# Optimization experiments

Measured on AMD Instinct MI355X. Metric: run time of the kernel, lower is better.

Reference implementation:

```python
import jax, jax.numpy as jnp
import numpy as np

B, N, DIN, H, DOUT = 32, 1024, 256, 256, 256
NEG = 9000000000000000.0  # -9e15 masking trick from the original code


def setup_inputs() -> dict:
    key = jax.random.key(0)
    ks = jax.random.split(key, 10)
    x = jax.random.normal(ks[0], (B, N, DIN), dtype=jnp.float32)
    # binary float mask (1 = edge present)
    mask = jax.random.randint(ks[1], (B, N, N), 0, 2).astype(jnp.float32)
    s = 0.02
    Wv = jax.random.normal(ks[2], (DIN, H), dtype=jnp.float32) * s
    bv = jnp.zeros((H,), jnp.float32)
    Wk = jax.random.normal(ks[3], (DIN, H), dtype=jnp.float32) * s
    bk = jnp.zeros((H,), jnp.float32)
    Wq = jax.random.normal(ks[4], (DIN, H), dtype=jnp.float32) * s
    bq = jnp.zeros((H,), jnp.float32)
    Wo = jax.random.normal(ks[5], (H, DOUT), dtype=jnp.float32) * s
    bo = jnp.zeros((DOUT,), jnp.float32)
    return {"x": x, "mask": mask, "Wv": Wv, "bv": bv, "Wk": Wk, "bk": bk,
            "Wq": Wq, "bq": bq, "Wo": Wo, "bo": bo}


def reference(x, mask, Wv, bv, Wk, bk, Wq, bq, Wo, bo):
    # x: [B,N,din], mask: [B,N,N]
    v = jax.nn.relu(x @ Wv + bv)              # [B,N,H]
    q = jax.nn.relu(x @ Wq + bq)              # [B,N,H]
    k = jax.nn.relu(x @ Wk + bk)              # [B,N,H]
    scores = jnp.einsum('bnh,bmh->bnm', q, k)  # QK^T, [B,N,N]
    att = jax.nn.softmax(scores * mask - NEG * (1.0 - mask), axis=-1)
    out = jnp.einsum('bnm,bmh->bnh', att, v)   # AV
    return jax.nn.relu(out @ Wo + bo)          # [B,N,d_out]
```

## Files before the change

kernel.cpp:

```cpp
#include <hip/hip_runtime.h>


typedef __attribute__((ext_vector_type(4))) float    f32x4;
typedef __attribute__((ext_vector_type(8))) short    s16x8;
typedef __attribute__((ext_vector_type(4))) short    s16x4;
typedef unsigned long long u64;

__device__ __forceinline__ short f2b(float f) {
    union { float f; unsigned u; } v; v.f = f;
    unsigned r = v.u + 0x7FFFu + ((v.u >> 16) & 1u);
    return (short)(r >> 16);
}

__device__ __forceinline__ void gl_lds16(const short* g, short* l) {
    __builtin_amdgcn_global_load_lds(
        (const __attribute__((address_space(1))) unsigned int*)g,
        (__attribute__((address_space(3))) unsigned int*)l, 16, 0, 0);
}

__global__ void prep_w(const float* __restrict__ Wq, const float* __restrict__ Wk,
                       const float* __restrict__ Wv, const float* __restrict__ Wo,
                       short* __restrict__ Wt) {
    int idx = blockIdx.x * 256 + threadIdx.x;
    int w = idx >> 16, rem = idx & 65535;
    int n = rem >> 8, kk = rem & 255;
    const float* W = (w == 0) ? Wq : (w == 1) ? Wk : (w == 2) ? Wv : Wo;
    Wt[idx] = f2b(W[kk * 256 + n]);
}

__global__ __launch_bounds__(256) void qkv_gemm(
        const float* __restrict__ x, const short* __restrict__ Wt,
        const float* __restrict__ bq, const float* __restrict__ bk, const float* __restrict__ bv,
        short* __restrict__ qO, short* __restrict__ kO, short* __restrict__ vtO) {
    __shared__ short a_lds[128][72];
    __shared__ short b_lds[3][64][72];
    const int tid = threadIdx.x;
    const int bm = blockIdx.x >> 2, bn = blockIdx.x & 3;
    const int s0 = bm * 128, n0 = bn * 64;
    const int wid = tid >> 6, l = tid & 63, lo4 = l & 15, hi4 = l >> 4;
    const int wm = wid >> 1, wn = wid & 1;

    f32x4 acc[3][4][2];
    #pragma unroll
    for (int w = 0; w < 3; ++w)
        #pragma unroll
        for (int mi = 0; mi < 4; ++mi)
            #pragma unroll
            for (int ni = 0; ni < 2; ++ni)
                acc[w][mi][ni] = (f32x4){0.f, 0.f, 0.f, 0.f};

    for (int kt = 0; kt < 4; ++kt) {
        const int k0 = kt * 64;
        #pragma unroll
        for (int i = 0; i < 8; ++i) {
            int ch = i * 256 + tid;
            int row = ch >> 4, c4 = (ch & 15) * 4;
            f32x4 xv = *(const f32x4*)(x + (size_t)(s0 + row) * 256 + k0 + c4);
            s16x4 pk = { f2b(xv.x), f2b(xv.y), f2b(xv.z), f2b(xv.w) };
            *(s16x4*)&a_lds[row][c4] = pk;
        }
        #pragma unroll
        for (int w = 0; w < 3; ++w) {
            #pragma unroll
            for (int i = 0; i < 2; ++i) {
                int ch = i * 256 + tid;
                int n = ch >> 3, c8 = (ch & 7) * 8;
                *(s16x8*)&b_lds[w][n][c8] =
                    *(const s16x8*)(Wt + (size_t)w * 65536 + (size_t)(n0 + n) * 256 + k0 + c8);
            }
        }
        __syncthreads();
        s16x8 af[4][2];
        #pragma unroll
        for (int mi = 0; mi < 4; ++mi)
            #pragma unroll
            for (int kk = 0; kk < 2; ++kk)
                af[mi][kk] = *(s16x8*)&a_lds[wm * 64 + mi * 16 + lo4][kk * 32 + hi4 * 8];
        #pragma unroll
        for (int w = 0; w < 3; ++w)
            #pragma unroll
            for (int ni = 0; ni < 2; ++ni)
                #pragma unroll
                for (int kk = 0; kk < 2; ++kk) {
                    s16x8 bfr = *(s16x8*)&b_lds[w][wn * 32 + ni * 16 + lo4][kk * 32 + hi4 * 8];
                    #pragma unroll
                    for (int mi = 0; mi < 4; ++mi)
                        acc[w][mi][ni] = __builtin_amdgcn_mfma_f32_16x16x32_bf16(
                            af[mi][kk], bfr, acc[w][mi][ni], 0, 0, 0);
                }
        __syncthreads();
    }

    const float* bias[3] = { bq, bk, bv };
    for (int w = 0; w < 3; ++w) {
        #pragma unroll
        for (int mi = 0; mi < 4; ++mi)
            #pragma unroll
            for (int ni = 0; ni < 2; ++ni)
                #pragma unroll
                for (int j = 0; j < 4; ++j) {
                    int r = wm * 64 + mi * 16 + hi4 * 4 + j;
                    int c = wn * 32 + ni * 16 + lo4;
                    float v = acc[w][mi][ni][j] + bias[w][n0 + c];
                    a_lds[r][c] = f2b(fmaxf(v, 0.f));
                }
        __syncthreads();
        if (w == 0) {
            #pragma unroll
            for (int i = 0; i < 4; ++i) {
                int ch = i * 256 + tid;
                int row = ch >> 3, c8 = (ch & 7) * 8;
                *(s16x8*)(qO + (size_t)(s0 + row) * 256 + n0 + c8) = *(s16x8*)&a_lds[row][c8];
            }
        } else if (w == 1) {
            #pragma unroll
            for (int i = 0; i < 4; ++i) {
                int ch = i * 256 + tid;
                int row = ch >> 3, c8 = (ch & 7) * 8;
                int swz = ((c8 >> 3) ^ (row & 7)) * 8;
                *(s16x8*)(kO + (size_t)(s0 + row) * 256 + n0 + swz) = *(s16x8*)&a_lds[row][c8];
            }
        } else {
            int bb = s0 >> 10, nn = s0 & 1023;
            #pragma unroll
            for (int i = 0; i < 4; ++i) {
                int ch = i * 256 + tid;
                int h = ch >> 4, sc = (ch & 15) * 8;
                s16x8 t;
                #pragma unroll
                for (int e = 0; e < 8; ++e) t[e] = a_lds[sc + e][h];
                int cil = sc >> 3;
                int swz = (cil & 8) | ((cil & 7) ^ ((n0 + h) & 7));
                *(s16x8*)(vtO + ((size_t)bb * 256 + n0 + h) * 1024 + nn + swz * 8) = t;
            }
        }
        __syncthreads();
    }
}

__global__ __launch_bounds__(512) void attn_fused(
        const short* __restrict__ q, const short* __restrict__ k,
        const short* __restrict__ vt, const float* __restrict__ mask,
        const short* __restrict__ WtO, const float* __restrict__ bo,
        float* __restrict__ out) {
    __shared__ short SM[65536];
    __shared__ short p_lds[8][16][72];
    const int tid = threadIdx.x, wid = tid >> 6, l = tid & 63;
    const int lo4 = l & 15, hi4 = l >> 4;
    const int bid = blockIdx.x;
    const int swz = (bid & 7) * 32 + (bid >> 3);
    const int b = swz >> 3, qb = swz & 7;
    const int q0 = qb * 128 + wid * 16;
    const size_t bq0 = (size_t)b * 1024 + qb * 128;
    const size_t bq_row = (size_t)b * 1024 + q0;

    const short* kb  = k  + (size_t)b * 1024 * 256;
    const short* vtg = vt + (size_t)b * 256 * 1024;
    const float* mtb = mask + bq_row * 1024;

#define KBUF(bufi) (SM + (bufi) * 16384)
#define VBUF(bufi) (SM + 32768 + (bufi) * 16384)
#define STAGE_K(bufi, c0_) do { const short* sg_ = kb + (size_t)(c0_) * 256;          \
    _Pragma("unroll") for (int i_ = 0; i_ < 4; ++i_) { int cb_ = i_ * 512 + wid * 64; \
        gl_lds16(sg_ + (size_t)(cb_ + l) * 8, KBUF(bufi) + cb_ * 8); } } while (0)
#define STAGE_V(bufi, c0_) do {                                                       \
    _Pragma("unroll") for (int i_ = 0; i_ < 4; ++i_) { int cb_ = i_ * 512 + wid * 64; \
        int ch_ = cb_ + l; int h_ = ch_ >> 3, cc_ = ch_ & 7;                          \
        gl_lds16(vtg + (size_t)h_ * 1024 + (c0_) + cc_ * 8, VBUF(bufi) + cb_ * 8); } } while (0)
#define LOAD_MASK(dst, c0_) do {                                                      \
    _Pragma("unroll") for (int i_ = 0; i_ < 4; ++i_)                                  \
        dst[i_] = *(const f32x4*)(mtb + (size_t)(i_ * 4 + hi4) * 1024 + (c0_) + lo4 * 4); } while (0)

    s16x8 qf[8];
    {
        const short* qp = q + (bq_row + lo4) * 256 + hi4 * 8;
        #pragma unroll
        for (int t = 0; t < 8; ++t) qf[t] = *(const s16x8*)(qp + t * 32);
    }
    f32x4 oacc[16];
    #pragma unroll
    for (int t = 0; t < 16; ++t) oacc[t] = (f32x4){0.f, 0.f, 0.f, 0.f};
    float m_run[4] = { -1e30f, -1e30f, -1e30f, -1e30f };
    float l_run[4] = { 0.f, 0.f, 0.f, 0.f };
    f32x4 mk0[4], mk1[4], mk2[4];

    LOAD_MASK(mk0, 0);
    STAGE_K(0, 0);
    STAGE_V(0, 0);
    LOAD_MASK(mk1, 64);

    for (int t = 0; t < 16; ++t) {
        const int cur = t & 1;
        const int c0 = t * 64;
        if (t < 15) {
            STAGE_K(cur ^ 1, c0 + 64);
            asm volatile("s_waitcnt vmcnt(12)" ::: "memory");
        } else {
            asm volatile("s_waitcnt vmcnt(4)" ::: "memory");
        }
        __builtin_amdgcn_s_barrier();
        f32x4 s[4];
        #pragma unroll
        for (int ct = 0; ct < 4; ++ct) s[ct] = (f32x4){0.f, 0.f, 0.f, 0.f};
        __builtin_amdgcn_s_setprio(1);
        #pragma unroll
        for (int ct = 0; ct < 4; ++ct) {
            int row = ct * 16 + lo4, rx = row & 7;
            #pragma unroll
            for (int tt = 0; tt < 8; ++tt) {
                int ch = tt * 4 + hi4;
                int sc = (ch & 24) | ((ch & 7) ^ rx);
                s16x8 kf = *(s16x8*)(KBUF(cur) + row * 256 + sc * 8);
                s[ct] = __builtin_amdgcn_mfma_f32_16x16x32_bf16(qf[tt], kf, s[ct], 0, 0, 0);
            }
        }
        __builtin_amdgcn_s_setprio(0);
        u64 bw[4][4];
        #pragma unroll
        for (int i = 0; i < 4; ++i) {
            bw[i][0] = __ballot(mk0[i].x != 0.f);
            bw[i][1] = __ballot(mk0[i].y != 0.f);
            bw[i][2] = __ballot(mk0[i].z != 0.f);
            bw[i][3] = __ballot(mk0[i].w != 0.f);
        }
        const int cc = lo4 & 3;
        u64 w0 = (cc == 0) ? bw[0][0] : (cc == 1) ? bw[0][1] : (cc == 2) ? bw[0][2] : bw[0][3];
        u64 w1 = (cc == 0) ? bw[1][0] : (cc == 1) ? bw[1][1] : (cc == 2) ? bw[1][2] : bw[1][3];
        u64 w2 = (cc == 0) ? bw[2][0] : (cc == 1) ? bw[2][1] : (cc == 2) ? bw[2][2] : bw[2][3];
        u64 w3 = (cc == 0) ? bw[3][0] : (cc == 1) ? bw[3][1] : (cc == 2) ? bw[3][2] : bw[3][3];
        u64 wsel = (hi4 == 0) ? w0 : (hi4 == 1) ? w1 : (hi4 == 2) ? w2 : w3;
        const unsigned sh0 = (unsigned)(lo4 >> 2);
        float sm[4][4];
        #pragma unroll
        for (int j = 0; j < 4; ++j) {
            unsigned wsx = (unsigned)(wsel >> (j * 16 + sh0));
            sm[0][j] = (wsx & 1u)    ? s[0][j] : -1e30f;
            sm[1][j] = (wsx & 16u)   ? s[1][j] : -1e30f;
            sm[2][j] = (wsx & 256u)  ? s[2][j] : -1e30f;
            sm[3][j] = (wsx & 4096u) ? s[3][j] : -1e30f;
        }
        float scale[4], p[4][4];
        #pragma unroll
        for (int j = 0; j < 4; ++j) {
            float tmx = fmaxf(fmaxf(sm[0][j], sm[1][j]), fmaxf(sm[2][j], sm[3][j]));
            tmx = fmaxf(tmx, __shfl_xor(tmx, 1));
            tmx = fmaxf(tmx, __shfl_xor(tmx, 2));
            tmx = fmaxf(tmx, __shfl_xor(tmx, 4));
            tmx = fmaxf(tmx, __shfl_xor(tmx, 8));
            float mnew = fmaxf(m_run[j], tmx);
            scale[j] = __expf(m_run[j] - mnew);
            m_run[j] = mnew;
            float su = 0.f;
            #pragma unroll
            for (int ct = 0; ct < 4; ++ct) { p[ct][j] = __expf(sm[ct][j] - mnew); su += p[ct][j]; }
            su += __shfl_xor(su, 1);
            su += __shfl_xor(su, 2);
            su += __shfl_xor(su, 4);
            su += __shfl_xor(su, 8);
            l_run[j] = l_run[j] * scale[j] + su;
        }
        #pragma unroll
        for (int tt = 0; tt < 16; ++tt)
            #pragma unroll
            for (int j = 0; j < 4; ++j) oacc[tt][j] *= scale[j];
        #pragma unroll
        for (int ct = 0; ct < 4; ++ct)
            #pragma unroll
            for (int j = 0; j < 4; ++j)
                p_lds[wid][hi4 * 4 + j][ct * 16 + lo4] = f2b(p[ct][j]);
        asm volatile("s_waitcnt lgkmcnt(0)" ::: "memory");
        __builtin_amdgcn_sched_barrier(0);
        s16x8 pa0 = *(s16x8*)&p_lds[wid][lo4][hi4 * 8];
        s16x8 pa1 = *(s16x8*)&p_lds[wid][lo4][32 + hi4 * 8];
        if (t < 15) {
            STAGE_V(cur ^ 1, c0 + 64);
            if (t < 14) {
                LOAD_MASK(mk2, c0 + 128);
                asm volatile("s_waitcnt vmcnt(16)" ::: "memory");
            } else {
                asm volatile("s_waitcnt vmcnt(12)" ::: "memory");
            }
        } else {
            asm volatile("s_waitcnt vmcnt(0)" ::: "memory");
        }
        __builtin_amdgcn_s_barrier();
        __builtin_amdgcn_s_setprio(1);
        #pragma unroll
        for (int nt = 0; nt < 16; ++nt) {
            int h = nt * 16 + lo4, hx = h & 7;
            s16x8 vf0 = *(s16x8*)(VBUF(cur) + h * 64 + (hi4 ^ hx) * 8);
            s16x8 vf1 = *(s16x8*)(VBUF(cur) + h * 64 + ((hi4 + 4) ^ hx) * 8);
            oacc[nt] = __builtin_amdgcn_mfma_f32_16x16x32_bf16(pa0, vf0, oacc[nt], 0, 0, 0);
            oacc[nt] = __builtin_amdgcn_mfma_f32_16x16x32_bf16(pa1, vf1, oacc[nt], 0, 0, 0);
        }
        __builtin_amdgcn_s_setprio(0);
        if (t < 15) {
            #pragma unroll
            for (int i = 0; i < 4; ++i) { mk0[i] = mk1[i]; mk1[i] = mk2[i]; }
        }
    }
    __syncthreads();

    float inv[4];
    #pragma unroll
    for (int j = 0; j < 4; ++j) inv[j] = 1.f / l_run[j];
    #pragma unroll
    for (int g = 0; g < 4; ++g) {
        asm volatile("s_waitcnt lgkmcnt(0)" ::: "memory");
        #pragma unroll
        for (int ntl = 0; ntl < 4; ++ntl)
            #pragma unroll
            for (int j = 0; j < 4; ++j)
                p_lds[wid][hi4 * 4 + j][ntl * 16 + lo4] = f2b(oacc[g * 4 + ntl][j] * inv[j]);
        asm volatile("s_waitcnt lgkmcnt(0)" ::: "memory");
        __builtin_amdgcn_sched_barrier(0);
        s16x8 r0 = *(s16x8*)&p_lds[wid][lo4][hi4 * 16];
        s16x8 r1 = *(s16x8*)&p_lds[wid][lo4][hi4 * 16 + 8];
        int arow = wid * 16 + lo4;
        *(s16x8*)&SM[arow * 264 + g * 64 + hi4 * 16]     = r0;
        *(s16x8*)&SM[arow * 264 + g * 64 + hi4 * 16 + 8] = r1;
    }
    short* wo = SM + 33792;
    #pragma unroll
    for (int i = 0; i < 4; ++i) {
        int idx = i * 512 + tid;
        int n = idx >> 5, c8 = (idx & 31) * 8;
        *(s16x8*)&wo[n * 264 + c8] = *(const s16x8*)(WtO + (size_t)n * 256 + c8);
    }
    __syncthreads();

    for (int chk = 0; chk < 4; ++chk) {
        const int n0 = chk * 64;
        f32x4 acc2[4];
        #pragma unroll
        for (int ni = 0; ni < 4; ++ni) acc2[ni] = (f32x4){0.f, 0.f, 0.f, 0.f};
        #pragma unroll
        for (int kk = 0; kk < 8; ++kk) {
            s16x8 af = *(s16x8*)&SM[(wid * 16 + lo4) * 264 + kk * 32 + hi4 * 8];
            #pragma unroll
            for (int ni = 0; ni < 4; ++ni) {
                s16x8 bf = *(s16x8*)&wo[(ni * 16 + lo4) * 264 + kk * 32 + hi4 * 8];
                acc2[ni] = __builtin_amdgcn_mfma_f32_16x16x32_bf16(af, bf, acc2[ni], 0, 0, 0);
            }
        }
        #pragma unroll
        for (int ni = 0; ni < 4; ++ni) {
            float bv = bo[n0 + ni * 16 + lo4];
            #pragma unroll
            for (int j = 0; j < 4; ++j) {
                int r = wid * 16 + hi4 * 4 + j;
                out[(bq0 + r) * 256 + n0 + ni * 16 + lo4] = fmaxf(acc2[ni][j] + bv, 0.f);
            }
        }
        if (chk < 3) {
            __syncthreads();
            #pragma unroll
            for (int i = 0; i < 4; ++i) {
                int idx = i * 512 + tid;
                int n = idx >> 5, c8 = (idx & 31) * 8;
                *(s16x8*)&wo[n * 264 + c8] =
                    *(const s16x8*)(WtO + (size_t)(n0 + 64 + n) * 256 + c8);
            }
            __syncthreads();
        }
    }
#undef KBUF
#undef VBUF
#undef STAGE_K
#undef STAGE_V
#undef LOAD_MASK
}

extern "C" void kernel_launch(void* const* d_in, const int* in_sizes, int n_in,
                              void* d_out, int out_size, void* d_ws, size_t ws_size,
                              hipStream_t stream) {
    const float* x    = (const float*)d_in[0];
    const float* mask = (const float*)d_in[1];
    const float* Wv   = (const float*)d_in[2];
    const float* bv   = (const float*)d_in[3];
    const float* Wk   = (const float*)d_in[4];
    const float* bk   = (const float*)d_in[5];
    const float* Wq   = (const float*)d_in[6];
    const float* bq   = (const float*)d_in[7];
    const float* Wo   = (const float*)d_in[8];
    const float* bo   = (const float*)d_in[9];
    float* out = (float*)d_out;

    char* ws = (char*)d_ws;
    short* Wt   = (short*)ws;
    short* qB   = (short*)(ws + (1 << 20));
    short* kB   = qB  + (size_t)32768 * 256;
    short* vtB  = kB  + (size_t)32768 * 256;
    (void)in_sizes; (void)n_in; (void)out_size; (void)ws_size;

    prep_w<<<1024, 256, 0, stream>>>(Wq, Wk, Wv, Wo, Wt);
    qkv_gemm<<<1024, 256, 0, stream>>>(x, Wt, bq, bk, bv, qB, kB, vtB);
    attn_fused<<<256, 512, 0, stream>>>(qB, kB, vtB, mask, Wt + 3 * 65536, bo, out);
}
```

Before: 125.1 us.

## Halve attention block size and single-buffer K/V to raise occupancy

```diff
diff --git a/kernel.cpp b/kernel.cpp
--- a/kernel.cpp
+++ b/kernel.cpp
@@ -138,38 +138,43 @@
     }
 }
 
-__global__ __launch_bounds__(512) void attn_fused(
+__global__ __launch_bounds__(256) void attn_fused(
         const short* __restrict__ q, const short* __restrict__ k,
         const short* __restrict__ vt, const float* __restrict__ mask,
         const short* __restrict__ WtO, const float* __restrict__ bo,
         float* __restrict__ out) {
-    __shared__ short SM[65536];
-    __shared__ short p_lds[8][16][72];
+    __shared__ short kbuf[16384];
+    __shared__ short vbuf[16384];
+    __shared__ short p_lds[4][16][72];
     const int tid = threadIdx.x, wid = tid >> 6, l = tid & 63;
     const int lo4 = l & 15, hi4 = l >> 4;
     const int bid = blockIdx.x;
-    const int swz = (bid & 7) * 32 + (bid >> 3);
-    const int b = swz >> 3, qb = swz & 7;
-    const int q0 = qb * 128 + wid * 16;
-    const size_t bq0 = (size_t)b * 1024 + qb * 128;
+    const int swz = (bid & 7) * 64 + (bid >> 3);
+    const int b = swz >> 4, qb = swz & 15;
+    const int q0 = qb * 64 + wid * 16;
+    const size_t bq0 = (size_t)b * 1024 + qb * 64;
     const size_t bq_row = (size_t)b * 1024 + q0;
 
     const short* kb  = k  + (size_t)b * 1024 * 256;
     const short* vtg = vt + (size_t)b * 256 * 1024;
     const float* mtb = mask + bq_row * 1024;
 
-#define KBUF(bufi) (SM + (bufi) * 16384)
-#define VBUF(bufi) (SM + 32768 + (bufi) * 16384)
-#define STAGE_K(bufi, c0_) do { const short* sg_ = kb + (size_t)(c0_) * 256;          \
-    _Pragma("unroll") for (int i_ = 0; i_ < 4; ++i_) { int cb_ = i_ * 512 + wid * 64; \
-        gl_lds16(sg_ + (size_t)(cb_ + l) * 8, KBUF(bufi) + cb_ * 8); } } while (0)
-#define STAGE_V(bufi, c0_) do {                                                       \
-    _Pragma("unroll") for (int i_ = 0; i_ < 4; ++i_) { int cb_ = i_ * 512 + wid * 64; \
+#define STAGE_K(c0_) do { const short* sg_ = kb + (size_t)(c0_) * 256;                \
+    _Pragma("unroll") for (int i_ = 0; i_ < 8; ++i_) { int cb_ = i_ * 256 + wid * 64; \
+        gl_lds16(sg_ + (size_t)(cb_ + l) * 8, kbuf + cb_ * 8); } } while (0)
+#define STAGE_V(c0_) do {                                                             \
+    _Pragma("unroll") for (int i_ = 0; i_ < 8; ++i_) { int cb_ = i_ * 256 + wid * 64; \
         int ch_ = cb_ + l; int h_ = ch_ >> 3, cc_ = ch_ & 7;                          \
-        gl_lds16(vtg + (size_t)h_ * 1024 + (c0_) + cc_ * 8, VBUF(bufi) + cb_ * 8); } } while (0)
+        gl_lds16(vtg + (size_t)h_ * 1024 + (c0_) + cc_ * 8, vbuf + cb_ * 8); } } while (0)
 #define LOAD_MASK(dst, c0_) do {                                                      \
     _Pragma("unroll") for (int i_ = 0; i_ < 4; ++i_)                                  \
         dst[i_] = *(const f32x4*)(mtb + (size_t)(i_ * 4 + hi4) * 1024 + (c0_) + lo4 * 4); } while (0)
+
+    f32x4 mk0[4], mk1[4], mk2[4];
+    LOAD_MASK(mk0, 0);
+    STAGE_K(0);
+    STAGE_V(0);
+    LOAD_MASK(mk1, 64);
 
     s16x8 qf[8];
     {
@@ -182,22 +187,11 @@
     for (int t = 0; t < 16; ++t) oacc[t] = (f32x4){0.f, 0.f, 0.f, 0.f};
     float m_run[4] = { -1e30f, -1e30f, -1e30f, -1e30f };
     float l_run[4] = { 0.f, 0.f, 0.f, 0.f };
-    f32x4 mk0[4], mk1[4], mk2[4];
-
-    LOAD_MASK(mk0, 0);
-    STAGE_K(0, 0);
-    STAGE_V(0, 0);
-    LOAD_MASK(mk1, 64);
 
     for (int t = 0; t < 16; ++t) {
-        const int cur = t & 1;
         const int c0 = t * 64;
-        if (t < 15) {
-            STAGE_K(cur ^ 1, c0 + 64);
-            asm volatile("s_waitcnt vmcnt(12)" ::: "memory");
-        } else {
-            asm volatile("s_waitcnt vmcnt(4)" ::: "memory");
-        }
+        if (t < 15) { asm volatile("s_waitcnt vmcnt(4)" ::: "memory"); }
+        else        { asm volatile("s_waitcnt vmcnt(0)" ::: "memory"); }
         __builtin_amdgcn_s_barrier();
         f32x4 s[4];
         #pragma unroll
@@ -210,11 +204,13 @@
             for (int tt = 0; tt < 8; ++tt) {
                 int ch = tt * 4 + hi4;
                 int sc = (ch & 24) | ((ch & 7) ^ rx);
-                s16x8 kf = *(s16x8*)(KBUF(cur) + row * 256 + sc * 8);
+                s16x8 kf = *(s16x8*)&kbuf[row * 256 + sc * 8];
                 s[ct] = __builtin_amdgcn_mfma_f32_16x16x32_bf16(qf[tt], kf, s[ct], 0, 0, 0);
             }
         }
         __builtin_amdgcn_s_setprio(0);
+        __builtin_amdgcn_s_barrier();
+        if (t < 15) STAGE_K(c0 + 64);
         u64 bw[4][4];
         #pragma unroll
         for (int i = 0; i < 4; ++i) {
@@ -272,38 +268,29 @@
         __builtin_amdgcn_sched_barrier(0);
         s16x8 pa0 = *(s16x8*)&p_lds[wid][lo4][hi4 * 8];
         s16x8 pa1 = *(s16x8*)&p_lds[wid][lo4][32 + hi4 * 8];
-        if (t < 15) {
-            STAGE_V(cur ^ 1, c0 + 64);
-            if (t < 14) {
-                LOAD_MASK(mk2, c0 + 128);
-                asm volatile("s_waitcnt vmcnt(16)" ::: "memory");
-            } else {
-                asm volatile("s_waitcnt vmcnt(12)" ::: "memory");
-            }
-        } else {
-            asm volatile("s_waitcnt vmcnt(0)" ::: "memory");
-        }
-        __builtin_amdgcn_s_barrier();
         __builtin_amdgcn_s_setprio(1);
         #pragma unroll
         for (int nt = 0; nt < 16; ++nt) {
             int h = nt * 16 + lo4, hx = h & 7;
-            s16x8 vf0 = *(s16x8*)(VBUF(cur) + h * 64 + (hi4 ^ hx) * 8);
-            s16x8 vf1 = *(s16x8*)(VBUF(cur) + h * 64 + ((hi4 + 4) ^ hx) * 8);
+            s16x8 vf0 = *(s16x8*)&vbuf[h * 64 + (hi4 ^ hx) * 8];
+            s16x8 vf1 = *(s16x8*)&vbuf[h * 64 + ((hi4 + 4) ^ hx) * 8];
             oacc[nt] = __builtin_amdgcn_mfma_f32_16x16x32_bf16(pa0, vf0, oacc[nt], 0, 0, 0);
             oacc[nt] = __builtin_amdgcn_mfma_f32_16x16x32_bf16(pa1, vf1, oacc[nt], 0, 0, 0);
         }
         __builtin_amdgcn_s_setprio(0);
+        __builtin_amdgcn_s_barrier();
         if (t < 15) {
+            STAGE_V(c0 + 64);
+            if (t < 14) LOAD_MASK(mk2, c0 + 128);
             #pragma unroll
             for (int i = 0; i < 4; ++i) { mk0[i] = mk1[i]; mk1[i] = mk2[i]; }
         }
     }
-    __syncthreads();
 
     float inv[4];
     #pragma unroll
     for (int j = 0; j < 4; ++j) inv[j] = 1.f / l_run[j];
+    s16x8 af2[8];
     #pragma unroll
     for (int g = 0; g < 4; ++g) {
         asm volatile("s_waitcnt lgkmcnt(0)" ::: "memory");
@@ -314,58 +301,45 @@
                 p_lds[wid][hi4 * 4 + j][ntl * 16 + lo4] = f2b(oacc[g * 4 + ntl][j] * inv[j]);
         asm volatile("s_waitcnt lgkmcnt(0)" ::: "memory");
         __builtin_amdgcn_sched_barrier(0);
-        s16x8 r0 = *(s16x8*)&p_lds[wid][lo4][hi4 * 16];
-        s16x8 r1 = *(s16x8*)&p_lds[wid][lo4][hi4 * 16 + 8];
-        int arow = wid * 16 + lo4;
-        *(s16x8*)&SM[arow * 264 + g * 64 + hi4 * 16]     = r0;
-        *(s16x8*)&SM[arow * 264 + g * 64 + hi4 * 16 + 8] = r1;
-    }
-    short* wo = SM + 33792;
-    #pragma unroll
-    for (int i = 0; i < 4; ++i) {
-        int idx = i * 512 + tid;
-        int n = idx >> 5, c8 = (idx & 31) * 8;
-        *(s16x8*)&wo[n * 264 + c8] = *(const s16x8*)(WtO + (size_t)n * 256 + c8);
-    }
-    __syncthreads();
+        af2[g * 2]     = *(s16x8*)&p_lds[wid][lo4][hi4 * 8];
+        af2[g * 2 + 1] = *(s16x8*)&p_lds[wid][lo4][32 + hi4 * 8];
+    }
+    asm volatile("s_waitcnt lgkmcnt(0)" ::: "memory");
 
     for (int chk = 0; chk < 4; ++chk) {
-        const int n0 = chk * 64;
+        __syncthreads();
+        #pragma unroll
+        for (int i = 0; i < 8; ++i) {
+            int idx = i * 256 + tid;
+            int n = idx >> 5, cil = idx & 31;
+            int scil = (cil & 24) | ((cil & 7) ^ (n & 7));
+            *(s16x8*)&vbuf[n * 256 + scil * 8] =
+                *(const s16x8*)(WtO + (size_t)(chk * 64 + n) * 256 + cil * 8);
+        }
+        __syncthreads();
         f32x4 acc2[4];
         #pragma unroll
         for (int ni = 0; ni < 4; ++ni) acc2[ni] = (f32x4){0.f, 0.f, 0.f, 0.f};
         #pragma unroll
         for (int kk = 0; kk < 8; ++kk) {
-            s16x8 af = *(s16x8*)&SM[(wid * 16 + lo4) * 264 + kk * 32 + hi4 * 8];
             #pragma unroll
             for (int ni = 0; ni < 4; ++ni) {
-                s16x8 bf = *(s16x8*)&wo[(ni * 16 + lo4) * 264 + kk * 32 + hi4 * 8];
-                acc2[ni] = __builtin_amdgcn_mfma_f32_16x16x32_bf16(af, bf, acc2[ni], 0, 0, 0);
+                int n = ni * 16 + lo4, ch = kk * 4 + hi4;
+                int sc = (ch & 24) | ((ch & 7) ^ (n & 7));
+                s16x8 bf = *(s16x8*)&vbuf[n * 256 + sc * 8];
+                acc2[ni] = __builtin_amdgcn_mfma_f32_16x16x32_bf16(af2[kk], bf, acc2[ni], 0, 0, 0);
             }
         }
         #pragma unroll
         for (int ni = 0; ni < 4; ++ni) {
-            float bv = bo[n0 + ni * 16 + lo4];
+            float bv = bo[chk * 64 + ni * 16 + lo4];
             #pragma unroll
             for (int j = 0; j < 4; ++j) {
                 int r = wid * 16 + hi4 * 4 + j;
-                out[(bq0 + r) * 256 + n0 + ni * 16 + lo4] = fmaxf(acc2[ni][j] + bv, 0.f);
-            }
-        }
-        if (chk < 3) {
-            __syncthreads();
-            #pragma unroll
-            for (int i = 0; i < 4; ++i) {
-                int idx = i * 512 + tid;
-                int n = idx >> 5, c8 = (idx & 31) * 8;
-                *(s16x8*)&wo[n * 264 + c8] =
-                    *(const s16x8*)(WtO + (size_t)(n0 + 64 + n) * 256 + c8);
-            }
-            __syncthreads();
-        }
-    }
-#undef KBUF
-#undef VBUF
+                out[(bq0 + r) * 256 + chk * 64 + ni * 16 + lo4] = fmaxf(acc2[ni][j] + bv, 0.f);
+            }
+        }
+    }
 #undef STAGE_K
 #undef STAGE_V
 #undef LOAD_MASK
@@ -395,5 +369,5 @@
 
     prep_w<<<1024, 256, 0, stream>>>(Wq, Wk, Wv, Wo, Wt);
     qkv_gemm<<<1024, 256, 0, stream>>>(x, Wt, bq, bk, bv, qB, kB, vtB);
-    attn_fused<<<256, 512, 0, stream>>>(qB, kB, vtB, mask, Wt + 3 * 65536, bo, out);
-}
+    attn_fused<<<512, 256, 0, stream>>>(qB, kB, vtB, mask, Wt + 3 * 65536, bo, out);
+}
```

Measured after the change: 179.9 us. 43.8% more time.
